# Performance work log

Measured on AMD Instinct MI355X. Metric: run time of the kernel, lower is better.

The kernel has to match this reference:

```python
import jax, jax.numpy as jnp
import numpy as np

T = 16384
D_HIDDEN = 1024
D_MODEL = 1024


def setup_inputs() -> dict:
    key = jax.random.key(0)
    k_in, k_nu, k_B, k_C, k_D = jax.random.split(key, 5)
    inputs = jax.random.normal(k_in, (T, D_MODEL), dtype=jnp.float32)
    # param inits mirror the flax module: uniform(-1,1)/sqrt(d_model) for nu_log,
    # normal/sqrt(d_model) for B, normal/sqrt(d_hidden) for C, normal for D.
    nu_log = jax.random.uniform(k_nu, (D_HIDDEN,), dtype=jnp.float32, minval=-1.0, maxval=1.0) / jnp.sqrt(jnp.float32(D_MODEL))
    B = jax.random.normal(k_B, (D_HIDDEN, D_MODEL), dtype=jnp.float32) / jnp.sqrt(jnp.float32(D_MODEL))
    C = jax.random.normal(k_C, (D_MODEL, D_HIDDEN), dtype=jnp.float32) / jnp.sqrt(jnp.float32(D_HIDDEN))
    Dp = jax.random.normal(k_D, (D_MODEL,), dtype=jnp.float32)
    return {"inputs": inputs, "nu_log": nu_log, "B": B, "C": C, "Dp": Dp}


def _binop(q_i, q_j):
    # composition of affine maps h -> a*h + b with diagonal a
    a_i, b_i = q_i
    a_j, b_j = q_j
    return (a_j * a_i, a_j * b_i + b_j)


def reference(inputs, nu_log, B, C, Dp):
    # h_t = lambda * h_{t-1} + B @ x_t ; y_t = C @ h_t + D * x_t
    t = inputs.shape[0]
    Lambda_elems = jnp.broadcast_to(nu_log[None, :], (t, nu_log.shape[0]))  # [T, H]
    Bu_elems = jnp.einsum('td,hd->th', inputs, B)  # [T, H]
    _, hidden = jax.lax.associative_scan(_binop, (Lambda_elems, Bu_elems))
    outputs = jnp.einsum('th,dh->td', hidden, C) + Dp[None, :] * inputs  # [T, D]
    return outputs
```

## Files before the change

kernel.cpp:

```cpp
#include <hip/hip_runtime.h>
#include <hip/hip_bf16.h>
#include <stdint.h>

typedef __attribute__((ext_vector_type(8))) __bf16 bf16x8;
typedef __attribute__((ext_vector_type(4))) float  f32x4;
typedef unsigned short ushort_t;

#define MFMA16(a, b, c) __builtin_amdgcn_mfma_f32_16x16x32_bf16((a), (b), (c), 0, 0, 0)

__device__ __forceinline__ ushort_t f2b(float f) {
    union { float f; uint32_t u; } v; v.f = f;
    uint32_t r = v.u + 0x7FFFu + ((v.u >> 16) & 1u);
    return (ushort_t)(r >> 16);
}
__device__ __forceinline__ float b2f(ushort_t u) {
    union { uint32_t u; float f; } v; v.u = (uint32_t)u << 16;
    return v.f;
}

#define GLDS16(g, l)                                                          \
    __builtin_amdgcn_global_load_lds(                                         \
        (const __attribute__((address_space(1))) void*)(g),                   \
        (__attribute__((address_space(3))) void*)(l), 16, 0, 0)

__global__ __launch_bounds__(256) void cvt3(const float* __restrict__ X, ushort_t* __restrict__ Xb,
                                            const float* __restrict__ B, ushort_t* __restrict__ Bb,
                                            const float* __restrict__ C, ushort_t* __restrict__ Cb) {
    const int b = blockIdx.x;
    const float* src; ushort_t* dst; int base;
    if (b < 16384)      { src = X; dst = Xb; base = b; }
    else if (b < 17408) { src = B; dst = Bb; base = b - 16384; }
    else                { src = C; dst = Cb; base = b - 17408; }
    const int idx = (base * 256 + threadIdx.x) * 4;
    float4 v = *(const float4*)&src[idx];
    ushort4 o;
    o.x = f2b(v.x); o.y = f2b(v.y); o.z = f2b(v.z); o.w = f2b(v.w);
    *(ushort4*)&dst[idx] = o;
}

__global__ __launch_bounds__(512, 2) void gemm1_scan(const ushort_t* __restrict__ A,
                                                     const ushort_t* __restrict__ W,
                                                     ushort_t* __restrict__ Hb,
                                                     int M, int N, int K,
                                                     const float* __restrict__ nu_log) {
    constexpr int BK = 64;
    extern __shared__ char smem[];
    __shared__ ushort_t wstrip[16 * 256];
    __shared__ char     wabuf[2][2048];

    const int tid  = threadIdx.x;
    const int lane = tid & 63;
    const int w    = tid >> 6;
    const int wm   = w >> 2;
    const int wn   = w & 3;

    const int nwg = gridDim.x;
    const int cpx = nwg >> 3;
    const int bid = (blockIdx.x & 7) * cpx + (blockIdx.x >> 3);
    const int nbn = N >> 8;
    const int row0 = (bid / nbn) << 8;
    const int col0 = (bid % nbn) << 8;
    const int NKT = K / BK;

    const int st_r = tid >> 3;
    const int g8   = ((tid & 7) ^ (st_r & 7)) * 8;
    const ushort_t* asrc[4];
    const ushort_t* bsrc[4];
#pragma unroll
    for (int j = 0; j < 4; ++j) {
        asrc[j] = A + (size_t)(row0 + j * 64 + st_r) * K + g8;
        bsrc[j] = W + (size_t)(col0 + j * 64 + st_r) * K + g8;
    }
    const int st_lds = tid * 16;

    const int st_rw = tid >> 3;
    const int g8w   = ((tid & 7) ^ (st_rw & 7)) * 8;
    const ushort_t* wsrc = A + (size_t)(row0 - 16 + st_rw) * K + g8w;

#define STAGE(buf, kt) {                                                      \
    char* _la = smem + (buf) * 65536;                                         \
    char* _lb = _la + 32768;                                                  \
    const int _ko = (kt) * BK;                                                \
    _Pragma("unroll")                                                         \
    for (int j = 0; j < 4; ++j) {                                             \
        GLDS16(asrc[j] + _ko, _la + j * 8192 + st_lds);                       \
        GLDS16(bsrc[j] + _ko, _lb + j * 8192 + st_lds);                       \
    }                                                                         \
    if (row0 && w < 2) GLDS16(wsrc + _ko, &wabuf[buf][0] + tid * 16); }

    const int l15 = lane & 15;
    const int l7  = lane & 7;
    const int ch  = lane >> 4;
    const int aoff0 = (wm * 128 + l15) * 128 + ((ch ^ l7) << 4);
    const int boff0 = (wn * 64  + l15) * 128 + ((ch ^ l7) << 4);
    const int woff0 = l15 * 128 + ((ch ^ l7) << 4);
    const int kxw   = (w & 1) << 6;

    f32x4 acc[8][4] = {};
    f32x4 acc_w[4] = {};
    const bool do_w = (wm == 0) && row0;

    STAGE(0, 0);
    asm volatile("s_waitcnt vmcnt(0)" ::: "memory");
    __builtin_amdgcn_s_barrier();

    int cur = 0;
    for (int kt = 0; kt < NKT; ++kt) {
        if (kt + 1 < NKT) STAGE(cur ^ 1, kt + 1);
        const char* sa = smem + cur * 65536;
        const char* sb = sa + 32768;
#pragma unroll
        for (int s = 0; s < 2; ++s) {
            const int kx = (s << 6) ^ kxw;
            bf16x8 bfr[4], afr[8];
#pragma unroll
            for (int n = 0; n < 4; ++n)
                bfr[n] = *(const bf16x8*)(sb + (boff0 ^ kx) + n * 2048);
#pragma unroll
            for (int m = 0; m < 8; ++m)
                afr[m] = *(const bf16x8*)(sa + (aoff0 ^ kx) + m * 2048);
            __builtin_amdgcn_s_setprio(1);
#pragma unroll
            for (int m = 0; m < 8; ++m)
#pragma unroll
                for (int n = 0; n < 4; ++n)
                    acc[m][n] = MFMA16(afr[m], bfr[n], acc[m][n]);
            __builtin_amdgcn_s_setprio(0);
            if (do_w) {
                bf16x8 awf = *(const bf16x8*)(&wabuf[cur][0] + (woff0 ^ kx));
#pragma unroll
                for (int n = 0; n < 4; ++n) acc_w[n] = MFMA16(awf, bfr[n], acc_w[n]);
            }
        }
        asm volatile("s_waitcnt vmcnt(0)" ::: "memory");
        __builtin_amdgcn_s_barrier();
        cur ^= 1;
    }
#undef STAGE

    const int fr = l15;
    const int fq = lane >> 4;
    ushort_t* cl = (ushort_t*)smem;
#pragma unroll
    for (int m = 0; m < 8; ++m)
#pragma unroll
        for (int n = 0; n < 4; ++n) {
            const int col = wn * 64 + n * 16 + fr;
#pragma unroll
            for (int r = 0; r < 4; ++r)
                cl[(wm * 128 + m * 16 + fq * 4 + r) * 256 + col] = f2b(acc[m][n][r]);
        }
    if (do_w) {
#pragma unroll
        for (int n = 0; n < 4; ++n) {
            const int col = wn * 64 + n * 16 + fr;
#pragma unroll
            for (int r = 0; r < 4; ++r)
                wstrip[(fq * 4 + r) * 256 + col] = f2b(acc_w[n][r]);
        }
    }
    __syncthreads();

    const int c0 = lane * 4;
    const float4 nu4 = *(const float4*)&nu_log[col0 + c0];
    float cr0 = 0.f, cr1 = 0.f, cr2 = 0.f, cr3 = 0.f;
#define SCAN_STEP(pu)                                                        \
    {   uint2 _v = (pu);                                                     \
        cr0 = fmaf(nu4.x, cr0, b2f((ushort_t)(_v.x & 0xffff)));              \
        cr1 = fmaf(nu4.y, cr1, b2f((ushort_t)(_v.x >> 16)));                 \
        cr2 = fmaf(nu4.z, cr2, b2f((ushort_t)(_v.y & 0xffff)));              \
        cr3 = fmaf(nu4.w, cr3, b2f((ushort_t)(_v.y >> 16))); }
    if (w == 0) {
        if (row0) {
#pragma unroll
            for (int t = 0; t < 16; ++t)
                SCAN_STEP(*(const uint2*)&wstrip[t * 256 + c0]);
        }
    } else {
#pragma unroll
        for (int t = 0; t < 16; ++t)
            SCAN_STEP(*(const uint2*)&cl[(w * 32 - 16 + t) * 256 + c0]);
    }
#pragma unroll
    for (int t = 0; t < 32; ++t) {
        SCAN_STEP(*(const uint2*)&cl[(w * 32 + t) * 256 + c0]);
        ushort4 o;
        o.x = f2b(cr0); o.y = f2b(cr1); o.z = f2b(cr2); o.w = f2b(cr3);
        *(ushort4*)&Hb[(size_t)(row0 + w * 32 + t) * N + col0 + c0] = o;
    }
#undef SCAN_STEP
}

__global__ __launch_bounds__(512, 2) void gemm2ph(const ushort_t* __restrict__ A,
                                                  const ushort_t* __restrict__ W,
                                                  float* __restrict__ Cout,
                                                  int M, int N, int K,
                                                  const ushort_t* __restrict__ Xres,
                                                  const float* __restrict__ Dp) {
    constexpr int BK = 64;
    extern __shared__ char smem[];

    const int tid  = threadIdx.x;
    const int lane = tid & 63;
    const int w    = tid >> 6;
    const int wm   = w >> 2;
    const int wn   = w & 3;

    const int nwg = gridDim.x;
    const int cpx = nwg >> 3;
    const int bid = (blockIdx.x & 7) * cpx + (blockIdx.x >> 3);
    const int nbn = N >> 8;
    const int row0 = (bid / nbn) << 8;
    const int col0 = (bid % nbn) << 8;
    const int NKT = K / BK;

    const int st_r = tid >> 3;
    const int g8   = ((tid & 7) ^ (st_r & 7)) * 8;
    const ushort_t* asrc[4];
    const ushort_t* bsrc[4];
#pragma unroll
    for (int j = 0; j < 4; ++j) {
        asrc[j] = A + (size_t)(row0 + j * 64 + st_r) * K + g8;
        bsrc[j] = W + (size_t)(col0 + j * 64 + st_r) * K + g8;
    }
    const int st_lds = tid * 16;

#define STAGE(buf, kt) {                                                      \
    char* _la = smem + (buf) * 65536;                                         \
    char* _lb = _la + 32768;                                                  \
    const int _ko = (kt) * BK;                                                \
    _Pragma("unroll")                                                         \
    for (int j = 0; j < 4; ++j) {                                             \
        GLDS16(asrc[j] + _ko, _la + j * 8192 + st_lds);                       \
        GLDS16(bsrc[j] + _ko, _lb + j * 8192 + st_lds);                       \
    } }

    const int l15 = lane & 15;
    const int l7  = lane & 7;
    const int ch  = lane >> 4;
    const int aoff0 = (wm * 128 + l15) * 128 + ((ch ^ l7) << 4);
    const int boff0 = (wn * 64  + l15) * 128 + ((ch ^ l7) << 4);
    const int kxw   = (w & 1) << 6;

    f32x4 acc[8][4] = {};

    STAGE(0, 0);
    asm volatile("s_waitcnt vmcnt(0)" ::: "memory");
    __builtin_amdgcn_s_barrier();

    int cur = 0;
    for (int kt = 0; kt < NKT; ++kt) {
        if (kt + 1 < NKT) STAGE(cur ^ 1, kt + 1);
        const char* sa = smem + cur * 65536;
        const char* sb = sa + 32768;
#pragma unroll
        for (int s = 0; s < 2; ++s) {
            const int kx = (s << 6) ^ kxw;
            bf16x8 bfr[4], afr[8];
#pragma unroll
            for (int n = 0; n < 4; ++n)
                bfr[n] = *(const bf16x8*)(sb + (boff0 ^ kx) + n * 2048);
#pragma unroll
            for (int m = 0; m < 8; ++m)
                afr[m] = *(const bf16x8*)(sa + (aoff0 ^ kx) + m * 2048);
            __builtin_amdgcn_s_setprio(1);
#pragma unroll
            for (int m = 0; m < 8; ++m)
#pragma unroll
                for (int n = 0; n < 4; ++n)
                    acc[m][n] = MFMA16(afr[m], bfr[n], acc[m][n]);
            __builtin_amdgcn_s_setprio(0);
        }
        asm volatile("s_waitcnt vmcnt(0)" ::: "memory");
        __builtin_amdgcn_s_barrier();
        cur ^= 1;
    }
#undef STAGE

    const int fr = l15;
    const int fq = lane >> 4;
    float* clf = (float*)smem;
#pragma unroll
    for (int h = 0; h < 2; ++h) {
        if (h) __builtin_amdgcn_s_barrier();
        if (wm == h) {
#pragma unroll
            for (int m = 0; m < 8; ++m)
#pragma unroll
                for (int n = 0; n < 4; ++n) {
                    const int col = wn * 64 + n * 16 + fr;
#pragma unroll
                    for (int r = 0; r < 4; ++r)
                        clf[(m * 16 + fq * 4 + r) * 256 + col] = acc[m][n][r];
                }
        }
        __builtin_amdgcn_s_barrier();
#pragma unroll
        for (int i = 0; i < 16; ++i) {
            const int q  = i * 512 + tid;
            const int rr = q >> 6, cc = (q & 63) * 4;
            float4 v = *(const float4*)(clf + rr * 256 + cc);
            const size_t grow = (size_t)(row0 + h * 128 + rr);
            ushort4 xv = *(const ushort4*)(Xres + grow * N + col0 + cc);
            float4  dp = *(const float4*)(Dp + col0 + cc);
            v.x += dp.x * b2f(xv.x); v.y += dp.y * b2f(xv.y);
            v.z += dp.z * b2f(xv.z); v.w += dp.w * b2f(xv.w);
            *(float4*)(Cout + grow * N + col0 + cc) = v;
        }
    }
}

extern "C" void kernel_launch(void* const* d_in, const int* in_sizes, int n_in,
                              void* d_out, int out_size, void* d_ws, size_t ws_size,
                              hipStream_t stream) {
    const float* X  = (const float*)d_in[0];
    const float* nu = (const float*)d_in[1];
    const float* B  = (const float*)d_in[2];
    const float* C  = (const float*)d_in[3];
    const float* Dp = (const float*)d_in[4];
    float* out = (float*)d_out;

    const int T = 16384, H = 1024, D = 1024;

    char* ws = (char*)d_ws;
    ushort_t* Xb  = (ushort_t*)(ws);
    ushort_t* Bb  = (ushort_t*)(ws + ((size_t)32 << 20));
    ushort_t* Cb  = (ushort_t*)(ws + ((size_t)34 << 20));
    ushort_t* Hb  = (ushort_t*)(ws + ((size_t)36 << 20));

    (void)hipFuncSetAttribute((const void*)&gemm1_scan,
                              hipFuncAttributeMaxDynamicSharedMemorySize, 131072);
    (void)hipFuncSetAttribute((const void*)&gemm2ph,
                              hipFuncAttributeMaxDynamicSharedMemorySize, 131072);

    cvt3<<<16384 + 1024 + 1024, 256, 0, stream>>>(X, Xb, B, Bb, C, Cb);

    gemm1_scan<<<(T / 256) * (H / 256), 512, 131072, stream>>>(
        Xb, Bb, Hb, T, H, D, nu);

    gemm2ph<<<(T / 256) * (D / 256), 512, 131072, stream>>>(
        Hb, Cb, out, T, D, H, Xb, Dp);
}
```

Measured before the change: 100.4 us.

## Shrink GEMM tiles to 128x256, single-buffer LDS, raise occupancy to four blocks

Result: slower. 109.6 us (+9.1%).

```diff
diff --git a/kernel.cpp b/kernel.cpp
--- a/kernel.cpp
+++ b/kernel.cpp
@@ -38,105 +38,94 @@
     *(ushort4*)&dst[idx] = o;
 }
 
-__global__ __launch_bounds__(512, 2) void gemm1_scan(const ushort_t* __restrict__ A,
+__global__ __launch_bounds__(512, 4) void gemm1_scan(const ushort_t* __restrict__ A,
                                                      const ushort_t* __restrict__ W,
                                                      ushort_t* __restrict__ Hb,
                                                      int M, int N, int K,
                                                      const float* __restrict__ nu_log) {
-    constexpr int BK = 64;
     extern __shared__ char smem[];
+    __shared__ ushort_t wabuf[1024];
     __shared__ ushort_t wstrip[16 * 256];
-    __shared__ char     wabuf[2][2048];
 
     const int tid  = threadIdx.x;
     const int lane = tid & 63;
     const int w    = tid >> 6;
-    const int wm   = w >> 2;
-    const int wn   = w & 3;
 
     const int nwg = gridDim.x;
     const int cpx = nwg >> 3;
     const int bid = (blockIdx.x & 7) * cpx + (blockIdx.x >> 3);
     const int nbn = N >> 8;
-    const int row0 = (bid / nbn) << 8;
+    const int row0 = (bid / nbn) << 7;
     const int col0 = (bid % nbn) << 8;
-    const int NKT = K / BK;
+    const int NKT = K >> 6;
 
     const int st_r = tid >> 3;
     const int g8   = ((tid & 7) ^ (st_r & 7)) * 8;
-    const ushort_t* asrc[4];
+    const ushort_t* asrc0 = A + (size_t)(row0 +      st_r) * K + g8;
+    const ushort_t* asrc1 = A + (size_t)(row0 + 64 + st_r) * K + g8;
     const ushort_t* bsrc[4];
 #pragma unroll
-    for (int j = 0; j < 4; ++j) {
-        asrc[j] = A + (size_t)(row0 + j * 64 + st_r) * K + g8;
+    for (int j = 0; j < 4; ++j)
         bsrc[j] = W + (size_t)(col0 + j * 64 + st_r) * K + g8;
-    }
+    const ushort_t* wsrc = A + (size_t)(row0 - 16 + st_r) * K + g8;
     const int st_lds = tid * 16;
-
-    const int st_rw = tid >> 3;
-    const int g8w   = ((tid & 7) ^ (st_rw & 7)) * 8;
-    const ushort_t* wsrc = A + (size_t)(row0 - 16 + st_rw) * K + g8w;
-
-#define STAGE(buf, kt) {                                                      \
-    char* _la = smem + (buf) * 65536;                                         \
-    char* _lb = _la + 32768;                                                  \
-    const int _ko = (kt) * BK;                                                \
-    _Pragma("unroll")                                                         \
-    for (int j = 0; j < 4; ++j) {                                             \
-        GLDS16(asrc[j] + _ko, _la + j * 8192 + st_lds);                       \
-        GLDS16(bsrc[j] + _ko, _lb + j * 8192 + st_lds);                       \
-    }                                                                         \
-    if (row0 && w < 2) GLDS16(wsrc + _ko, &wabuf[buf][0] + tid * 16); }
 
     const int l15 = lane & 15;
     const int l7  = lane & 7;
     const int ch  = lane >> 4;
-    const int aoff0 = (wm * 128 + l15) * 128 + ((ch ^ l7) << 4);
-    const int boff0 = (wn * 64  + l15) * 128 + ((ch ^ l7) << 4);
+    const int aoff0 = l15 * 128 + ((ch ^ l7) << 4);
+    const int boff0 = 16384 + (w * 32 + l15) * 128 + ((ch ^ l7) << 4);
     const int woff0 = l15 * 128 + ((ch ^ l7) << 4);
-    const int kxw   = (w & 1) << 6;
-
-    f32x4 acc[8][4] = {};
-    f32x4 acc_w[4] = {};
-    const bool do_w = (wm == 0) && row0;
-
-    STAGE(0, 0);
-    asm volatile("s_waitcnt vmcnt(0)" ::: "memory");
-    __builtin_amdgcn_s_barrier();
-
-    int cur = 0;
+
+    f32x4 acc[8][2] = {};
+    f32x4 acc_w[2] = {};
+    const bool do_w = (row0 != 0);
+
     for (int kt = 0; kt < NKT; ++kt) {
-        if (kt + 1 < NKT) STAGE(cur ^ 1, kt + 1);
-        const char* sa = smem + cur * 65536;
-        const char* sb = sa + 32768;
-#pragma unroll
-        for (int s = 0; s < 2; ++s) {
-            const int kx = (s << 6) ^ kxw;
-            bf16x8 bfr[4], afr[8];
-#pragma unroll
-            for (int n = 0; n < 4; ++n)
-                bfr[n] = *(const bf16x8*)(sb + (boff0 ^ kx) + n * 2048);
-#pragma unroll
-            for (int m = 0; m < 8; ++m)
-                afr[m] = *(const bf16x8*)(sa + (aoff0 ^ kx) + m * 2048);
+        const size_t ko = (size_t)kt * 64;
+        GLDS16(asrc0 + ko, smem + st_lds);
+        GLDS16(asrc1 + ko, smem + 8192 + st_lds);
+#pragma unroll
+        for (int j = 0; j < 4; ++j)
+            GLDS16(bsrc[j] + ko, smem + 16384 + j * 8192 + st_lds);
+        if (do_w && tid < 128) GLDS16(wsrc + ko, (char*)wabuf + tid * 16);
+        __syncthreads();
+#pragma unroll
+        for (int kh = 0; kh < 2; ++kh) {
+            const int kx = kh << 6;
+            bf16x8 bfr[2], afr[4];
+#pragma unroll
+            for (int n = 0; n < 2; ++n)
+                bfr[n] = *(const bf16x8*)(smem + ((boff0 + n * 2048) ^ kx));
+#pragma unroll
+            for (int m = 0; m < 4; ++m)
+                afr[m] = *(const bf16x8*)(smem + ((aoff0 + m * 2048) ^ kx));
             __builtin_amdgcn_s_setprio(1);
 #pragma unroll
-            for (int m = 0; m < 8; ++m)
-#pragma unroll
-                for (int n = 0; n < 4; ++n)
+            for (int m = 0; m < 4; ++m)
+#pragma unroll
+                for (int n = 0; n < 2; ++n)
                     acc[m][n] = MFMA16(afr[m], bfr[n], acc[m][n]);
             __builtin_amdgcn_s_setprio(0);
+#pragma unroll
+            for (int m = 0; m < 4; ++m)
+                afr[m] = *(const bf16x8*)(smem + ((aoff0 + (m + 4) * 2048) ^ kx));
+            __builtin_amdgcn_s_setprio(1);
+#pragma unroll
+            for (int m = 0; m < 4; ++m)
+#pragma unroll
+                for (int n = 0; n < 2; ++n)
+                    acc[m + 4][n] = MFMA16(afr[m], bfr[n], acc[m + 4][n]);
+            __builtin_amdgcn_s_setprio(0);
             if (do_w) {
-                bf16x8 awf = *(const bf16x8*)(&wabuf[cur][0] + (woff0 ^ kx));
-#pragma unroll
-                for (int n = 0; n < 4; ++n) acc_w[n] = MFMA16(awf, bfr[n], acc_w[n]);
+                bf16x8 awf = *(const bf16x8*)((const char*)wabuf + (woff0 ^ kx));
+#pragma unroll
+                for (int n = 0; n < 2; ++n)
+                    acc_w[n] = MFMA16(awf, bfr[n], acc_w[n]);
             }
         }
-        asm volatile("s_waitcnt vmcnt(0)" ::: "memory");
-        __builtin_amdgcn_s_barrier();
-        cur ^= 1;
-    }
-#undef STAGE
+        __syncthreads();
+    }
 
     const int fr = l15;
     const int fq = lane >> 4;
@@ -144,16 +133,16 @@
 #pragma unroll
     for (int m = 0; m < 8; ++m)
 #pragma unroll
-        for (int n = 0; n < 4; ++n) {
-            const int col = wn * 64 + n * 16 + fr;
+        for (int n = 0; n < 2; ++n) {
+            const int col = w * 32 + n * 16 + fr;
 #pragma unroll
             for (int r = 0; r < 4; ++r)
-                cl[(wm * 128 + m * 16 + fq * 4 + r) * 256 + col] = f2b(acc[m][n][r]);
+                cl[(m * 16 + fq * 4 + r) * 256 + col] = f2b(acc[m][n][r]);
         }
     if (do_w) {
 #pragma unroll
-        for (int n = 0; n < 4; ++n) {
-            const int col = wn * 64 + n * 16 + fr;
+        for (int n = 0; n < 2; ++n) {
+            const int col = w * 32 + n * 16 + fr;
 #pragma unroll
             for (int r = 0; r < 4; ++r)
                 wstrip[(fq * 4 + r) * 256 + col] = f2b(acc_w[n][r]);
@@ -171,7 +160,7 @@
         cr2 = fmaf(nu4.z, cr2, b2f((ushort_t)(_v.y & 0xffff)));              \
         cr3 = fmaf(nu4.w, cr3, b2f((ushort_t)(_v.y >> 16))); }
     if (w == 0) {
-        if (row0) {
+        if (do_w) {
 #pragma unroll
             for (int t = 0; t < 16; ++t)
                 SCAN_STEP(*(const uint2*)&wstrip[t * 256 + c0]);
@@ -179,134 +168,109 @@
     } else {
 #pragma unroll
         for (int t = 0; t < 16; ++t)
-            SCAN_STEP(*(const uint2*)&cl[(w * 32 - 16 + t) * 256 + c0]);
-    }
-#pragma unroll
-    for (int t = 0; t < 32; ++t) {
-        SCAN_STEP(*(const uint2*)&cl[(w * 32 + t) * 256 + c0]);
+            SCAN_STEP(*(const uint2*)&cl[(w * 16 - 16 + t) * 256 + c0]);
+    }
+#pragma unroll
+    for (int t = 0; t < 16; ++t) {
+        SCAN_STEP(*(const uint2*)&cl[(w * 16 + t) * 256 + c0]);
         ushort4 o;
         o.x = f2b(cr0); o.y = f2b(cr1); o.z = f2b(cr2); o.w = f2b(cr3);
-        *(ushort4*)&Hb[(size_t)(row0 + w * 32 + t) * N + col0 + c0] = o;
+        *(ushort4*)&Hb[(size_t)(row0 + w * 16 + t) * N + col0 + c0] = o;
     }
 #undef SCAN_STEP
 }
 
-__global__ __launch_bounds__(512, 2) void gemm2ph(const ushort_t* __restrict__ A,
+__global__ __launch_bounds__(512, 4) void gemm2ph(const ushort_t* __restrict__ A,
                                                   const ushort_t* __restrict__ W,
                                                   float* __restrict__ Cout,
                                                   int M, int N, int K,
                                                   const ushort_t* __restrict__ Xres,
                                                   const float* __restrict__ Dp) {
-    constexpr int BK = 64;
     extern __shared__ char smem[];
 
     const int tid  = threadIdx.x;
     const int lane = tid & 63;
     const int w    = tid >> 6;
-    const int wm   = w >> 2;
-    const int wn   = w & 3;
 
     const int nwg = gridDim.x;
     const int cpx = nwg >> 3;
     const int bid = (blockIdx.x & 7) * cpx + (blockIdx.x >> 3);
     const int nbn = N >> 8;
-    const int row0 = (bid / nbn) << 8;
+    const int row0 = (bid / nbn) << 7;
     const int col0 = (bid % nbn) << 8;
-    const int NKT = K / BK;
+    const int NKT = K >> 6;
 
     const int st_r = tid >> 3;
     const int g8   = ((tid & 7) ^ (st_r & 7)) * 8;
-    const ushort_t* asrc[4];
+    const ushort_t* asrc0 = A + (size_t)(row0 +      st_r) * K + g8;
+    const ushort_t* asrc1 = A + (size_t)(row0 + 64 + st_r) * K + g8;
     const ushort_t* bsrc[4];
 #pragma unroll
-    for (int j = 0; j < 4; ++j) {
-        asrc[j] = A + (size_t)(row0 + j * 64 + st_r) * K + g8;
+    for (int j = 0; j < 4; ++j)
         bsrc[j] = W + (size_t)(col0 + j * 64 + st_r) * K + g8;
-    }
     const int st_lds = tid * 16;
-
-#define STAGE(buf, kt) {                                                      \
-    char* _la = smem + (buf) * 65536;                                         \
-    char* _lb = _la + 32768;                                                  \
-    const int _ko = (kt) * BK;                                                \
-    _Pragma("unroll")                                                         \
-    for (int j = 0; j < 4; ++j) {                                             \
-        GLDS16(asrc[j] + _ko, _la + j * 8192 + st_lds);                       \
-        GLDS16(bsrc[j] + _ko, _lb + j * 8192 + st_lds);                       \
-    } }
 
     const int l15 = lane & 15;
     const int l7  = lane & 7;
     const int ch  = lane >> 4;
-    const int aoff0 = (wm * 128 + l15) * 128 + ((ch ^ l7) << 4);
-    const int boff0 = (wn * 64  + l15) * 128 + ((ch ^ l7) << 4);
-    const int kxw   = (w & 1) << 6;
-
-    f32x4 acc[8][4] = {};
-
-    STAGE(0, 0);
-    asm volatile("s_waitcnt vmcnt(0)" ::: "memory");
-    __builtin_amdgcn_s_barrier();
-
-    int cur = 0;
+    const int aoff0 = l15 * 128 + ((ch ^ l7) << 4);
+    const int boff0 = 16384 + (w * 32 + l15) * 128 + ((ch ^ l7) << 4);
+
+    f32x4 acc[8][2] = {};
+
     for (int kt = 0; kt < NKT; ++kt) {
-        if (kt + 1 < NKT) STAGE(cur ^ 1, kt + 1);
-        const char* sa = smem + cur * 65536;
-        const char* sb = sa + 32768;
-#pragma unroll
-        for (int s = 0; s < 2; ++s) {
-            const int kx = (s << 6) ^ kxw;
-            bf16x8 bfr[4], afr[8];
-#pragma unroll
-            for (int n = 0; n < 4; ++n)
-                bfr[n] = *(const bf16x8*)(sb + (boff0 ^ kx) + n * 2048);
-#pragma unroll
-            for (int m = 0; m < 8; ++m)
-                afr[m] = *(const bf16x8*)(sa + (aoff0 ^ kx) + m * 2048);
+        const size_t ko = (size_t)kt * 64;
+        GLDS16(asrc0 + ko, smem + st_lds);
+        GLDS16(asrc1 + ko, smem + 8192 + st_lds);
+#pragma unroll
+        for (int j = 0; j < 4; ++j)
+            GLDS16(bsrc[j] + ko, smem + 16384 + j * 8192 + st_lds);
+        __syncthreads();
+#pragma unroll
+        for (int kh = 0; kh < 2; ++kh) {
+            const int kx = kh << 6;
+            bf16x8 bfr[2], afr[4];
+#pragma unroll
+            for (int n = 0; n < 2; ++n)
+                bfr[n] = *(const bf16x8*)(smem + ((boff0 + n * 2048) ^ kx));
+#pragma unroll
+            for (int m = 0; m < 4; ++m)
+                afr[m] = *(const bf16x8*)(smem + ((aoff0 + m * 2048) ^ kx));
             __builtin_amdgcn_s_setprio(1);
 #pragma unroll
-            for (int m = 0; m < 8; ++m)
-#pragma unroll
-                for (int n = 0; n < 4; ++n)
+            for (int m = 0; m < 4; ++m)
+#pragma unroll
+                for (int n = 0; n < 2; ++n)
                     acc[m][n] = MFMA16(afr[m], bfr[n], acc[m][n]);
             __builtin_amdgcn_s_setprio(0);
-        }
-        asm volatile("s_waitcnt vmcnt(0)" ::: "memory");
-        __builtin_amdgcn_s_barrier();
-        cur ^= 1;
-    }
-#undef STAGE
+#pragma unroll
+            for (int m = 0; m < 4; ++m)
+                afr[m] = *(const bf16x8*)(smem + ((aoff0 + (m + 4) * 2048) ^ kx));
+            __builtin_amdgcn_s_setprio(1);
+#pragma unroll
+            for (int m = 0; m < 4; ++m)
+#pragma unroll
+                for (int n = 0; n < 2; ++n)
+                    acc[m + 4][n] = MFMA16(afr[m], bfr[n], acc[m + 4][n]);
+            __builtin_amdgcn_s_setprio(0);
+        }
+        __syncthreads();
+    }
 
     const int fr = l15;
     const int fq = lane >> 4;
-    float* clf = (float*)smem;
-#pragma unroll
-    for (int h = 0; h < 2; ++h) {
-        if (h) __builtin_amdgcn_s_barrier();
-        if (wm == h) {
-#pragma unroll
-            for (int m = 0; m < 8; ++m)
-#pragma unroll
-                for (int n = 0; n < 4; ++n) {
-                    const int col = wn * 64 + n * 16 + fr;
-#pragma unroll
-                    for (int r = 0; r < 4; ++r)
-                        clf[(m * 16 + fq * 4 + r) * 256 + col] = acc[m][n][r];
-                }
-        }
-        __builtin_amdgcn_s_barrier();
-#pragma unroll
-        for (int i = 0; i < 16; ++i) {
-            const int q  = i * 512 + tid;
-            const int rr = q >> 6, cc = (q & 63) * 4;
-            float4 v = *(const float4*)(clf + rr * 256 + cc);
-            const size_t grow = (size_t)(row0 + h * 128 + rr);
-            ushort4 xv = *(const ushort4*)(Xres + grow * N + col0 + cc);
-            float4  dp = *(const float4*)(Dp + col0 + cc);
-            v.x += dp.x * b2f(xv.x); v.y += dp.y * b2f(xv.y);
-            v.z += dp.z * b2f(xv.z); v.w += dp.w * b2f(xv.w);
-            *(float4*)(Cout + grow * N + col0 + cc) = v;
-        }
+#pragma unroll
+    for (int n = 0; n < 2; ++n) {
+        const int col = col0 + w * 32 + n * 16 + fr;
+        const float dpc = Dp[col];
+#pragma unroll
+        for (int m = 0; m < 8; ++m)
+#pragma unroll
+            for (int r = 0; r < 4; ++r) {
+                const int row = row0 + m * 16 + fq * 4 + r;
+                Cout[(size_t)row * N + col] =
+                    acc[m][n][r] + dpc * b2f(Xres[(size_t)row * N + col]);
+            }
     }
 }
 
@@ -329,15 +293,15 @@
     ushort_t* Hb  = (ushort_t*)(ws + ((size_t)36 << 20));
 
     (void)hipFuncSetAttribute((const void*)&gemm1_scan,
-                              hipFuncAttributeMaxDynamicSharedMemorySize, 131072);
+                              hipFuncAttributeMaxDynamicSharedMemorySize, 65536);
     (void)hipFuncSetAttribute((const void*)&gemm2ph,
-                              hipFuncAttributeMaxDynamicSharedMemorySize, 131072);
+                              hipFuncAttributeMaxDynamicSharedMemorySize, 49152);
 
     cvt3<<<16384 + 1024 + 1024, 256, 0, stream>>>(X, Xb, B, Bb, C, Cb);
 
-    gemm1_scan<<<(T / 256) * (H / 256), 512, 131072, stream>>>(
+    gemm1_scan<<<(T / 128) * (H / 256), 512, 65536, stream>>>(
         Xb, Bb, Hb, T, H, D, nu);
 
-    gemm2ph<<<(T / 256) * (D / 256), 512, 131072, stream>>>(
+    gemm2ph<<<(T / 128) * (D / 256), 512, 49152, stream>>>(
         Hb, Cb, out, T, D, H, Xb, Dp);
 }
```

## Fuse X fp32-to-bf16 conversion into GEMM1 A-tile staging via registers

Applied to the files above, without the earlier changes.

New measurement: 158.3 us. 1.58x slower.

```diff
diff --git a/kernel.cpp b/kernel.cpp
--- a/kernel.cpp
+++ b/kernel.cpp
@@ -17,20 +17,21 @@
     union { uint32_t u; float f; } v; v.u = (uint32_t)u << 16;
     return v.f;
 }
+__device__ __forceinline__ uint32_t pk2(float lo, float hi) {
+    return (uint32_t)f2b(lo) | ((uint32_t)f2b(hi) << 16);
+}
 
 #define GLDS16(g, l)                                                          \
     __builtin_amdgcn_global_load_lds(                                         \
         (const __attribute__((address_space(1))) void*)(g),                   \
         (__attribute__((address_space(3))) void*)(l), 16, 0, 0)
 
-__global__ __launch_bounds__(256) void cvt3(const float* __restrict__ X, ushort_t* __restrict__ Xb,
-                                            const float* __restrict__ B, ushort_t* __restrict__ Bb,
+__global__ __launch_bounds__(256) void cvt2(const float* __restrict__ B, ushort_t* __restrict__ Bb,
                                             const float* __restrict__ C, ushort_t* __restrict__ Cb) {
     const int b = blockIdx.x;
     const float* src; ushort_t* dst; int base;
-    if (b < 16384)      { src = X; dst = Xb; base = b; }
-    else if (b < 17408) { src = B; dst = Bb; base = b - 16384; }
-    else                { src = C; dst = Cb; base = b - 17408; }
+    if (b < 1024) { src = B; dst = Bb; base = b; }
+    else          { src = C; dst = Cb; base = b - 1024; }
     const int idx = (base * 256 + threadIdx.x) * 4;
     float4 v = *(const float4*)&src[idx];
     ushort4 o;
@@ -38,7 +39,7 @@
     *(ushort4*)&dst[idx] = o;
 }
 
-__global__ __launch_bounds__(512, 2) void gemm1_scan(const ushort_t* __restrict__ A,
+__global__ __launch_bounds__(512, 2) void gemm1_scan(const float* __restrict__ Xf,
                                                      const ushort_t* __restrict__ W,
                                                      ushort_t* __restrict__ Hb,
                                                      int M, int N, int K,
@@ -46,7 +47,7 @@
     constexpr int BK = 64;
     extern __shared__ char smem[];
     __shared__ ushort_t wstrip[16 * 256];
-    __shared__ char     wabuf[2][2048];
+    __shared__ ushort_t wabuf[2][1024];
 
     const int tid  = threadIdx.x;
     const int lane = tid & 63;
@@ -64,29 +65,52 @@
 
     const int st_r = tid >> 3;
     const int g8   = ((tid & 7) ^ (st_r & 7)) * 8;
-    const ushort_t* asrc[4];
+    const float*    asrcf[4];
     const ushort_t* bsrc[4];
 #pragma unroll
     for (int j = 0; j < 4; ++j) {
-        asrc[j] = A + (size_t)(row0 + j * 64 + st_r) * K + g8;
-        bsrc[j] = W + (size_t)(col0 + j * 64 + st_r) * K + g8;
+        asrcf[j] = Xf + (size_t)(row0 + j * 64 + st_r) * K + g8;
+        bsrc[j]  = W  + (size_t)(col0 + j * 64 + st_r) * K + g8;
     }
     const int st_lds = tid * 16;
-
-    const int st_rw = tid >> 3;
-    const int g8w   = ((tid & 7) ^ (st_rw & 7)) * 8;
-    const ushort_t* wsrc = A + (size_t)(row0 - 16 + st_rw) * K + g8w;
-
-#define STAGE(buf, kt) {                                                      \
-    char* _la = smem + (buf) * 65536;                                         \
-    char* _lb = _la + 32768;                                                  \
+    const float* wsrcf = Xf + (size_t)(row0 - 16 + st_r) * K + g8;
+
+    const bool do_w2 = (row0 != 0);
+    const bool do_w  = (wm == 0) && do_w2;
+
+    float4 av[4][2];
+    float4 wv[2];
+
+#define A_LOAD(kt) { const int _ko = (kt) * BK;                               \
+    _Pragma("unroll")                                                         \
+    for (int j = 0; j < 4; ++j) {                                             \
+        av[j][0] = *(const float4*)(asrcf[j] + _ko);                          \
+        av[j][1] = *(const float4*)(asrcf[j] + _ko + 4);                      \
+    }                                                                         \
+    if (do_w2 && tid < 128) {                                                 \
+        wv[0] = *(const float4*)(wsrcf + _ko);                                \
+        wv[1] = *(const float4*)(wsrcf + _ko + 4);                            \
+    } }
+#define B_STAGE(buf, kt) { char* _lb = smem + (buf) * 65536 + 32768;          \
     const int _ko = (kt) * BK;                                                \
     _Pragma("unroll")                                                         \
+    for (int j = 0; j < 4; ++j) GLDS16(bsrc[j] + _ko, _lb + j * 8192 + st_lds); }
+#define A_WRITE(buf) { char* _la = smem + (buf) * 65536;                      \
+    _Pragma("unroll")                                                         \
     for (int j = 0; j < 4; ++j) {                                             \
-        GLDS16(asrc[j] + _ko, _la + j * 8192 + st_lds);                       \
-        GLDS16(bsrc[j] + _ko, _lb + j * 8192 + st_lds);                       \
+        uint4 u;                                                              \
+        u.x = pk2(av[j][0].x, av[j][0].y);                                    \
+        u.y = pk2(av[j][0].z, av[j][0].w);                                    \
+        u.z = pk2(av[j][1].x, av[j][1].y);                                    \
+        u.w = pk2(av[j][1].z, av[j][1].w);                                    \
+        *(uint4*)(_la + j * 8192 + st_lds) = u;                               \
     }                                                                         \
-    if (row0 && w < 2) GLDS16(wsrc + _ko, &wabuf[buf][0] + tid * 16); }
+    if (do_w2 && tid < 128) {                                                 \
+        uint4 u;                                                              \
+        u.x = pk2(wv[0].x, wv[0].y);  u.y = pk2(wv[0].z, wv[0].w);            \
+        u.z = pk2(wv[1].x, wv[1].y);  u.w = pk2(wv[1].z, wv[1].w);            \
+        *(uint4*)((char*)&wabuf[buf][0] + tid * 16) = u;                      \
+    } }
 
     const int l15 = lane & 15;
     const int l7  = lane & 7;
@@ -94,24 +118,24 @@
     const int aoff0 = (wm * 128 + l15) * 128 + ((ch ^ l7) << 4);
     const int boff0 = (wn * 64  + l15) * 128 + ((ch ^ l7) << 4);
     const int woff0 = l15 * 128 + ((ch ^ l7) << 4);
-    const int kxw   = (w & 1) << 6;
 
     f32x4 acc[8][4] = {};
     f32x4 acc_w[4] = {};
-    const bool do_w = (wm == 0) && row0;
-
-    STAGE(0, 0);
+
+    A_LOAD(0);
+    B_STAGE(0, 0);
     asm volatile("s_waitcnt vmcnt(0)" ::: "memory");
-    __builtin_amdgcn_s_barrier();
+    A_WRITE(0);
+    __syncthreads();
 
     int cur = 0;
     for (int kt = 0; kt < NKT; ++kt) {
-        if (kt + 1 < NKT) STAGE(cur ^ 1, kt + 1);
+        if (kt + 1 < NKT) { A_LOAD(kt + 1); B_STAGE(cur ^ 1, kt + 1); }
         const char* sa = smem + cur * 65536;
         const char* sb = sa + 32768;
 #pragma unroll
         for (int s = 0; s < 2; ++s) {
-            const int kx = (s << 6) ^ kxw;
+            const int kx = s << 6;
             bf16x8 bfr[4], afr[8];
 #pragma unroll
             for (int n = 0; n < 4; ++n)
@@ -127,16 +151,19 @@
                     acc[m][n] = MFMA16(afr[m], bfr[n], acc[m][n]);
             __builtin_amdgcn_s_setprio(0);
             if (do_w) {
-                bf16x8 awf = *(const bf16x8*)(&wabuf[cur][0] + (woff0 ^ kx));
+                bf16x8 awf = *(const bf16x8*)((const char*)&wabuf[cur][0] + (woff0 ^ kx));
 #pragma unroll
                 for (int n = 0; n < 4; ++n) acc_w[n] = MFMA16(awf, bfr[n], acc_w[n]);
             }
         }
         asm volatile("s_waitcnt vmcnt(0)" ::: "memory");
-        __builtin_amdgcn_s_barrier();
+        if (kt + 1 < NKT) A_WRITE(cur ^ 1);
+        __syncthreads();
         cur ^= 1;
     }
-#undef STAGE
+#undef A_LOAD
+#undef B_STAGE
+#undef A_WRITE
 
     const int fr = l15;
     const int fq = lane >> 4;
@@ -171,7 +198,7 @@
         cr2 = fmaf(nu4.z, cr2, b2f((ushort_t)(_v.y & 0xffff)));              \
         cr3 = fmaf(nu4.w, cr3, b2f((ushort_t)(_v.y >> 16))); }
     if (w == 0) {
-        if (row0) {
+        if (do_w2) {
 #pragma unroll
             for (int t = 0; t < 16; ++t)
                 SCAN_STEP(*(const uint2*)&wstrip[t * 256 + c0]);
@@ -195,7 +222,7 @@
                                                   const ushort_t* __restrict__ W,
                                                   float* __restrict__ Cout,
                                                   int M, int N, int K,
-                                                  const ushort_t* __restrict__ Xres,
+                                                  const float* __restrict__ Xres,
                                                   const float* __restrict__ Dp) {
     constexpr int BK = 64;
     extern __shared__ char smem[];
@@ -240,7 +267,6 @@
     const int ch  = lane >> 4;
     const int aoff0 = (wm * 128 + l15) * 128 + ((ch ^ l7) << 4);
     const int boff0 = (wn * 64  + l15) * 128 + ((ch ^ l7) << 4);
-    const int kxw   = (w & 1) << 6;
 
     f32x4 acc[8][4] = {};
 
@@ -255,7 +281,7 @@
         const char* sb = sa + 32768;
 #pragma unroll
         for (int s = 0; s < 2; ++s) {
-            const int kx = (s << 6) ^ kxw;
+            const int kx = s << 6;
             bf16x8 bfr[4], afr[8];
 #pragma unroll
             for (int n = 0; n < 4; ++n)
@@ -301,10 +327,10 @@
             const int rr = q >> 6, cc = (q & 63) * 4;
             float4 v = *(const float4*)(clf + rr * 256 + cc);
             const size_t grow = (size_t)(row0 + h * 128 + rr);
-            ushort4 xv = *(const ushort4*)(Xres + grow * N + col0 + cc);
-            float4  dp = *(const float4*)(Dp + col0 + cc);
-            v.x += dp.x * b2f(xv.x); v.y += dp.y * b2f(xv.y);
-            v.z += dp.z * b2f(xv.z); v.w += dp.w * b2f(xv.w);
+            float4 xv = *(const float4*)(Xres + grow * N + col0 + cc);
+            float4 dp = *(const float4*)(Dp + col0 + cc);
+            v.x += dp.x * xv.x; v.y += dp.y * xv.y;
+            v.z += dp.z * xv.z; v.w += dp.w * xv.w;
             *(float4*)(Cout + grow * N + col0 + cc) = v;
         }
     }
@@ -323,21 +349,20 @@
     const int T = 16384, H = 1024, D = 1024;
 
     char* ws = (char*)d_ws;
-    ushort_t* Xb  = (ushort_t*)(ws);
-    ushort_t* Bb  = (ushort_t*)(ws + ((size_t)32 << 20));
-    ushort_t* Cb  = (ushort_t*)(ws + ((size_t)34 << 20));
-    ushort_t* Hb  = (ushort_t*)(ws + ((size_t)36 << 20));
+    ushort_t* Bb = (ushort_t*)(ws);
+    ushort_t* Cb = (ushort_t*)(ws + ((size_t)2 << 20));
+    ushort_t* Hb = (ushort_t*)(ws + ((size_t)4 << 20));
 
     (void)hipFuncSetAttribute((const void*)&gemm1_scan,
                               hipFuncAttributeMaxDynamicSharedMemorySize, 131072);
     (void)hipFuncSetAttribute((const void*)&gemm2ph,
                               hipFuncAttributeMaxDynamicSharedMemorySize, 131072);
 
-    cvt3<<<16384 + 1024 + 1024, 256, 0, stream>>>(X, Xb, B, Bb, C, Cb);
+    cvt2<<<2048, 256, 0, stream>>>(B, Bb, C, Cb);
 
     gemm1_scan<<<(T / 256) * (H / 256), 512, 131072, stream>>>(
-        Xb, Bb, Hb, T, H, D, nu);
+        X, Bb, Hb, T, H, D, nu);
 
     gemm2ph<<<(T / 256) * (D / 256), 512, 131072, stream>>>(
-        Hb, Cb, out, T, D, H, Xb, Dp);
-}
+        Hb, Cb, out, T, D, H, X, Dp);
+}
```
